# Kernel optimization log

Measured on AMD Instinct MI355X. Metric: run time of the kernel, lower is better.

## Reference

```python
import jax, jax.numpy as jnp
import numpy as np

D_MODEL = 1024
NUM_HEADS = 16
HEAD_DIM = D_MODEL // NUM_HEADS


def setup_inputs() -> dict:
    key = jax.random.key(0)
    k_x, k_wqkv, k_bqkv, k_wfc, k_bfc = jax.random.split(key, 5)
    scale_in = 1.0 / np.sqrt(D_MODEL)
    return {
        "x": jax.random.normal(k_x, (2, 2048, D_MODEL), dtype=jnp.float32),
        # torch nn.Linear stores weight as [out_features, in_features]
        "w_qkv": jax.random.uniform(k_wqkv, (3 * D_MODEL, D_MODEL), jnp.float32, -scale_in, scale_in),
        "b_qkv": jax.random.uniform(k_bqkv, (3 * D_MODEL,), jnp.float32, -scale_in, scale_in),
        "w_fc": jax.random.uniform(k_wfc, (D_MODEL, D_MODEL), jnp.float32, -scale_in, scale_in),
        "b_fc": jax.random.uniform(k_bfc, (D_MODEL,), jnp.float32, -scale_in, scale_in),
    }


def reference(x, w_qkv, b_qkv, w_fc, b_fc):
    B, S, _ = x.shape
    # fused QKV projection: [B,S,3*d_model]
    qkv = jnp.einsum("bsd,ed->bse", x, w_qkv) + b_qkv
    # [B,S,H,3*head_dim] -> [B,H,S,3*head_dim]
    qkv = qkv.reshape(B, S, NUM_HEADS, 3 * HEAD_DIM).transpose(0, 2, 1, 3)
    Q, K, V = jnp.split(qkv, 3, axis=-1)  # each [B,H,S,head_dim]
    scores = jnp.einsum("bhqd,bhkd->bhqk", Q, K) / np.sqrt(HEAD_DIM).astype(np.float32)
    attention = jax.nn.softmax(scores, axis=-1)  # [B,H,S,S]
    values = jnp.einsum("bhqk,bhkd->bhqd", attention, V)
    # [B,H,S,head_dim] -> [B,S,d_model]
    values = values.transpose(0, 2, 1, 3).reshape(B, S, D_MODEL)
    out = jnp.einsum("bsd,ed->bse", values, w_fc) + b_fc
    return out
```

## Files before the change

### kernel.cpp

```cpp
#include <hip/hip_runtime.h>
#include <hip/hip_bf16.h>

#define D_MODEL 1024
#define NH 16
#define HD 64
#define BATCH 2
#define SEQ 2048

typedef __attribute__((ext_vector_type(8))) short short8;
typedef __attribute__((ext_vector_type(4))) float floatx4;

static __device__ __forceinline__ short f2bf(float f) {
    __hip_bfloat16 h = __float2bfloat16(f);
    return *reinterpret_cast<short*>(&h);
}
static __device__ __forceinline__ unsigned int pk2bf(float a, float b) {
    float2 t; t.x = a; t.y = b;
    __hip_bfloat162 h2 = __float22bfloat162_rn(t);
    return *reinterpret_cast<unsigned int*>(&h2);
}

__global__ __launch_bounds__(256) void cvt_all(
    const float* __restrict__ x, const float* __restrict__ wq,
    const float* __restrict__ wf,
    short* __restrict__ Xb, short* __restrict__ Wqb, short* __restrict__ Wfb)
{
    int i = blockIdx.x * 256 + threadIdx.x;
    const float* src; short* dst; int off;
    if (i < 524288)      { src = x;  dst = Xb;  off = i; }
    else if (i < 917504) { src = wq; dst = Wqb; off = i - 524288; }
    else                 { src = wf; dst = Wfb; off = i - 917504; }
    float4 a = *reinterpret_cast<const float4*>(src + off * 8);
    float4 b = *reinterpret_cast<const float4*>(src + off * 8 + 4);
    short8 o;
    o[0] = f2bf(a.x); o[1] = f2bf(a.y); o[2] = f2bf(a.z); o[3] = f2bf(a.w);
    o[4] = f2bf(b.x); o[5] = f2bf(b.y); o[6] = f2bf(b.z); o[7] = f2bf(b.w);
    *reinterpret_cast<short8*>(dst + off * 8) = o;
}

__global__ __launch_bounds__(256) void qkv_gemm(
    const short* __restrict__ X, const short* __restrict__ W,
    const float* __restrict__ bias,
    short* __restrict__ Qs, short* __restrict__ Ks, short* __restrict__ Vt_g)
{
    __shared__ __align__(16) short As[128][72];
    __shared__ __align__(16) short Bs[64][72];
    const int tid = threadIdx.x;
    const int bx = blockIdx.x;
    const int m0 = blockIdx.y * 128;
    const int n0 = bx * 64;
    const int h = bx / 3, t = bx % 3;
    const int bi = m0 >> 11;
    const int sl0 = m0 & 2047;
    const int w = tid >> 6, lane = tid & 63;
    const int quad = lane >> 4, l15 = lane & 15;
    const int wm2 = w >> 1, wn2 = w & 1;

    floatx4 acc[4][2];
#pragma unroll
    for (int i = 0; i < 4; i++)
#pragma unroll
        for (int j = 0; j < 2; j++) acc[i][j] = (floatx4)0.0f;

    for (int k0 = 0; k0 < 1024; k0 += 64) {
        __syncthreads();
#pragma unroll
        for (int i = 0; i < 4; i++) {
            int c = tid + i * 256;
            int row = c >> 3, ck = c & 7;
            *reinterpret_cast<uint4*>(&As[row][ck * 8]) =
                *reinterpret_cast<const uint4*>(&X[(m0 + row) * 1024 + k0 + ck * 8]);
        }
#pragma unroll
        for (int i = 0; i < 2; i++) {
            int c = tid + i * 256;
            int row = c >> 3, ck = c & 7;
            *reinterpret_cast<uint4*>(&Bs[row][ck * 8]) =
                *reinterpret_cast<const uint4*>(&W[(n0 + row) * 1024 + k0 + ck * 8]);
        }
        __syncthreads();
#pragma unroll
        for (int kk = 0; kk < 2; kk++) {
            short8 a[4], b[2];
#pragma unroll
            for (int i = 0; i < 4; i++)
                a[i] = *reinterpret_cast<const short8*>(&As[wm2 * 64 + i * 16 + l15][kk * 32 + quad * 8]);
#pragma unroll
            for (int j = 0; j < 2; j++)
                b[j] = *reinterpret_cast<const short8*>(&Bs[wn2 * 32 + j * 16 + l15][kk * 32 + quad * 8]);
#pragma unroll
            for (int mt = 0; mt < 4; mt++)
#pragma unroll
                for (int nt = 0; nt < 2; nt++)
                    acc[mt][nt] = __builtin_amdgcn_mfma_f32_16x16x32_bf16(
                        a[mt], b[nt], acc[mt][nt], 0, 0, 0);
        }
    }

    __syncthreads();
    short* T = &As[0][0];
#pragma unroll
    for (int nt = 0; nt < 2; nt++) {
        int col = wn2 * 32 + nt * 16 + l15;
        float bv = bias[h * 192 + t * 64 + col];
#pragma unroll
        for (int mt = 0; mt < 4; mt++) {
#pragma unroll
            for (int r = 0; r < 4; r++) {
                int ml = wm2 * 64 + mt * 16 + quad * 4 + r;
                float v = acc[mt][nt][r] + bv;
                if (t == 0) v *= 0.125f;
                if (t < 2) As[ml][col] = f2bf(v);
                else       T[col * 136 + ml] = f2bf(v);
            }
        }
    }
    __syncthreads();

    if (t < 2) {
        short* dst = (t == 0) ? Qs : Ks;
#pragma unroll
        for (int i = 0; i < 4; i++) {
            int c = tid + i * 256;
            int row = c >> 3, ck = c & 7;
            uint4 u = *reinterpret_cast<const uint4*>(&As[row][ck * 8]);
            *reinterpret_cast<uint4*>(
                &dst[((size_t)(bi * NH + h) * SEQ + sl0 + row) * HD + ck * 8]) = u;
        }
    } else {
#pragma unroll
        for (int i = 0; i < 4; i++) {
            int c = tid + i * 256;
            int drow = c >> 4, ck = c & 15;
            uint4 u = *reinterpret_cast<const uint4*>(&T[drow * 136 + ck * 8]);
            *reinterpret_cast<uint4*>(
                &Vt_g[((size_t)(bi * NH + h) * HD + drow) * SEQ + sl0 + ck * 8]) = u;
        }
    }
}

__global__ __launch_bounds__(256) void attn_kernel(
    const short* __restrict__ Qs, const short* __restrict__ Ks,
    const short* __restrict__ Vt_g, short* __restrict__ attn)
{
    __shared__ __align__(16) char smem[64 * 72 * 2 * 2];
    __shared__ __align__(16) short Pl[4][32][40];
    __shared__ float Ls[2][64];

    short (*Kl)[72] = (short(*)[72])smem;
    short (*Vt)[72] = (short(*)[72])(smem + 64 * 72 * 2);
    float (*Osum)[66] = (float(*)[66])smem;

    const int tid = threadIdx.x;
    const int w = tid >> 6, lane = tid & 63;
    const int wq = w >> 1, wk = w & 1;
    const int quad = lane >> 4, l15 = lane & 15;
    const int q0 = blockIdx.x * 64;
    const int h = blockIdx.y, bi = blockIdx.z;
    const int bh = bi * NH + h;
    const int kbase = bh * SEQ * HD;
    const int vbase = bh * HD * SEQ;

    short8 aq[2][2];
#pragma unroll
    for (int qt2 = 0; qt2 < 2; qt2++) {
        const short* qp = Qs + kbase + (q0 + wq * 32 + qt2 * 16 + l15) * HD;
#pragma unroll
        for (int c = 0; c < 2; c++)
            aq[qt2][c] = *reinterpret_cast<const short8*>(qp + c * 32 + quad * 8);
    }

    float l_acc[2] = {0.f, 0.f};
    floatx4 o[2][4];
#pragma unroll
    for (int mt = 0; mt < 2; mt++)
#pragma unroll
        for (int nt = 0; nt < 4; nt++) o[mt][nt] = (floatx4)0.0f;

    for (int kt = 0; kt < SEQ; kt += 64) {
        __syncthreads();
#pragma unroll
        for (int i = 0; i < 2; i++) {
            int c = tid + i * 256;
            int row = c >> 3, ck = c & 7;
            *reinterpret_cast<uint4*>(&Kl[row][ck * 8]) =
                *reinterpret_cast<const uint4*>(&Ks[kbase + (kt + row) * HD + ck * 8]);
            *reinterpret_cast<uint4*>(&Vt[row][ck * 8]) =
                *reinterpret_cast<const uint4*>(&Vt_g[vbase + row * SEQ + kt + ck * 8]);
        }
        __syncthreads();

        floatx4 sf[2][2];
#pragma unroll
        for (int kt2 = 0; kt2 < 2; kt2++)
#pragma unroll
            for (int qt2 = 0; qt2 < 2; qt2++) sf[kt2][qt2] = (floatx4)0.0f;
#pragma unroll
        for (int c = 0; c < 2; c++) {
#pragma unroll
            for (int kt2 = 0; kt2 < 2; kt2++) {
                short8 bk = *reinterpret_cast<const short8*>(
                    &Kl[wk * 32 + kt2 * 16 + l15][c * 32 + quad * 8]);
#pragma unroll
                for (int qt2 = 0; qt2 < 2; qt2++)
                    sf[kt2][qt2] = __builtin_amdgcn_mfma_f32_16x16x32_bf16(
                        bk, aq[qt2][c], sf[kt2][qt2], 0, 0, 0);
            }
        }

#pragma unroll
        for (int kt2 = 0; kt2 < 2; kt2++) {
#pragma unroll
            for (int qt2 = 0; qt2 < 2; qt2++) {
                float e0 = __expf(sf[kt2][qt2][0]);
                float e1 = __expf(sf[kt2][qt2][1]);
                float e2 = __expf(sf[kt2][qt2][2]);
                float e3 = __expf(sf[kt2][qt2][3]);
                l_acc[qt2] += (e0 + e1) + (e2 + e3);
                uint2 p;
                p.x = pk2bf(e0, e1);
                p.y = pk2bf(e2, e3);
                *reinterpret_cast<uint2*>(&Pl[w][qt2 * 16 + l15][kt2 * 16 + quad * 4]) = p;
            }
        }
        asm volatile("s_waitcnt lgkmcnt(0)" ::: "memory");

#pragma unroll
        for (int mt = 0; mt < 2; mt++) {
            short8 ap = *reinterpret_cast<const short8*>(&Pl[w][mt * 16 + l15][quad * 8]);
#pragma unroll
            for (int nt = 0; nt < 4; nt++) {
                short8 bv = *reinterpret_cast<const short8*>(
                    &Vt[nt * 16 + l15][wk * 32 + quad * 8]);
                o[mt][nt] = __builtin_amdgcn_mfma_f32_16x16x32_bf16(
                    ap, bv, o[mt][nt], 0, 0, 0);
            }
        }
    }

#pragma unroll
    for (int qt2 = 0; qt2 < 2; qt2++) {
        l_acc[qt2] += __shfl_xor(l_acc[qt2], 16);
        l_acc[qt2] += __shfl_xor(l_acc[qt2], 32);
    }
    if (quad == 0) {
        Ls[wk][wq * 32 + l15]      = l_acc[0];
        Ls[wk][wq * 32 + 16 + l15] = l_acc[1];
    }
    __syncthreads();

    if (wk == 0) {
#pragma unroll
        for (int mt = 0; mt < 2; mt++)
#pragma unroll
            for (int nt = 0; nt < 4; nt++)
#pragma unroll
                for (int r = 0; r < 4; r++)
                    Osum[wq * 32 + mt * 16 + quad * 4 + r][nt * 16 + l15] = o[mt][nt][r];
    }
    __syncthreads();
    if (wk == 1) {
#pragma unroll
        for (int mt = 0; mt < 2; mt++) {
#pragma unroll
            for (int r = 0; r < 4; r++) {
                int qrow = wq * 32 + mt * 16 + quad * 4 + r;
                float lt = Ls[0][qrow] + Ls[1][qrow];
#pragma unroll
                for (int nt = 0; nt < 4; nt++) {
                    float val = (o[mt][nt][r] + Osum[qrow][nt * 16 + l15]) / lt;
                    attn[(bi * SEQ + q0 + qrow) * D_MODEL + h * HD + nt * 16 + l15] = f2bf(val);
                }
            }
        }
    }
}

__global__ __launch_bounds__(256) void fc_gemm(
    const short* __restrict__ A, const short* __restrict__ W,
    const float* __restrict__ bias, float* __restrict__ out)
{
    __shared__ __align__(16) short As[128][72];
    __shared__ __align__(16) short Bs[128][72];
    const int tid = threadIdx.x;
    const int m0 = blockIdx.y * 128;
    const int n0 = blockIdx.x * 128;
    const int w = tid >> 6, lane = tid & 63;
    const int quad = lane >> 4, l15 = lane & 15;
    const int wm = (w >> 1) * 64, wn = (w & 1) * 64;

    floatx4 acc[4][4];
#pragma unroll
    for (int i = 0; i < 4; i++)
#pragma unroll
        for (int j = 0; j < 4; j++) acc[i][j] = (floatx4)0.0f;

    for (int k0 = 0; k0 < 1024; k0 += 64) {
        __syncthreads();
#pragma unroll
        for (int i = 0; i < 4; i++) {
            int c = tid + i * 256;
            int row = c >> 3, ck = c & 7;
            *reinterpret_cast<uint4*>(&As[row][ck * 8]) =
                *reinterpret_cast<const uint4*>(&A[(m0 + row) * 1024 + k0 + ck * 8]);
            *reinterpret_cast<uint4*>(&Bs[row][ck * 8]) =
                *reinterpret_cast<const uint4*>(&W[(n0 + row) * 1024 + k0 + ck * 8]);
        }
        __syncthreads();
#pragma unroll
        for (int kk = 0; kk < 2; kk++) {
            short8 a[4], b[4];
#pragma unroll
            for (int t = 0; t < 4; t++) {
                a[t] = *reinterpret_cast<const short8*>(&As[wm + t * 16 + l15][kk * 32 + quad * 8]);
                b[t] = *reinterpret_cast<const short8*>(&Bs[wn + t * 16 + l15][kk * 32 + quad * 8]);
            }
#pragma unroll
            for (int mt = 0; mt < 4; mt++)
#pragma unroll
                for (int nt = 0; nt < 4; nt++)
                    acc[mt][nt] = __builtin_amdgcn_mfma_f32_16x16x32_bf16(
                        a[mt], b[nt], acc[mt][nt], 0, 0, 0);
        }
    }

#pragma unroll
    for (int nt = 0; nt < 4; nt++) {
        int col = n0 + wn + nt * 16 + l15;
        float bv = bias[col];
#pragma unroll
        for (int mt = 0; mt < 4; mt++) {
#pragma unroll
            for (int r = 0; r < 4; r++) {
                int row = m0 + wm + mt * 16 + quad * 4 + r;
                out[row * 1024 + col] = acc[mt][nt][r] + bv;
            }
        }
    }
}

extern "C" void kernel_launch(void* const* d_in, const int* in_sizes, int n_in,
                              void* d_out, int out_size, void* d_ws, size_t ws_size,
                              hipStream_t stream) {
    const float* x     = (const float*)d_in[0];
    const float* w_qkv = (const float*)d_in[1];
    const float* b_qkv = (const float*)d_in[2];
    const float* w_fc  = (const float*)d_in[3];
    const float* b_fc  = (const float*)d_in[4];
    float* out = (float*)d_out;

    const size_t M4 = 4u * 1024 * 1024;
    short* Xb    = (short*)d_ws;
    short* Wqb   = Xb + M4;
    short* Wfb   = Wqb + 3u * 1024 * 1024;
    short* Qs    = Wfb + 1024 * 1024;
    short* Ks    = Qs + M4;
    short* Vt_g  = Ks + M4;
    short* attnb = Xb;

    cvt_all<<<4096, 256, 0, stream>>>(x, w_qkv, w_fc, Xb, Wqb, Wfb);
    qkv_gemm<<<dim3(48, 32), 256, 0, stream>>>(Xb, Wqb, b_qkv, Qs, Ks, Vt_g);
    attn_kernel<<<dim3(32, 16, 2), 256, 0, stream>>>(Qs, Ks, Vt_g, attnb);
    fc_gemm<<<dim3(8, 32), 256, 0, stream>>>(attnb, Wfb, b_fc, out);
}
```

Baseline: 224.7 us.

## Give each attention warp full key range; halve fc_gemm N tile

The attention kernel now has each of the four warps own 32 query rows across the full 64-key tile, with 128 queries per block. This removes the split-K reduction across warp pairs through shared memory and its extra barriers, and halves the number of blocks so each K/V tile load is shared by twice as many queries. Separately, fc_gemm shrinks its N tile from 128 to 64, doubling the grid to 512 blocks to fill more CUs at the cost of reloading the A tiles more often. The attention change trades fewer blocks (512) and larger per-warp register and LDS use for less K/V traffic and simpler reduction.

```diff
diff --git a/kernel.cpp b/kernel.cpp
--- a/kernel.cpp
+++ b/kernel.cpp
@@ -143,19 +143,15 @@
     const short* __restrict__ Qs, const short* __restrict__ Ks,
     const short* __restrict__ Vt_g, short* __restrict__ attn)
 {
-    __shared__ __align__(16) char smem[64 * 72 * 2 * 2];
-    __shared__ __align__(16) short Pl[4][32][40];
-    __shared__ float Ls[2][64];
-
-    short (*Kl)[72] = (short(*)[72])smem;
-    short (*Vt)[72] = (short(*)[72])(smem + 64 * 72 * 2);
-    float (*Osum)[66] = (float(*)[66])smem;
+    __shared__ __align__(16) short Kl[64][72];
+    __shared__ __align__(16) short Vt[64][72];
+    __shared__ __align__(16) short Pl[4][32][72];
+    __shared__ float Ls[128];
 
     const int tid = threadIdx.x;
     const int w = tid >> 6, lane = tid & 63;
-    const int wq = w >> 1, wk = w & 1;
     const int quad = lane >> 4, l15 = lane & 15;
-    const int q0 = blockIdx.x * 64;
+    const int q0 = blockIdx.x * 128;
     const int h = blockIdx.y, bi = blockIdx.z;
     const int bh = bi * NH + h;
     const int kbase = bh * SEQ * HD;
@@ -164,7 +160,7 @@
     short8 aq[2][2];
 #pragma unroll
     for (int qt2 = 0; qt2 < 2; qt2++) {
-        const short* qp = Qs + kbase + (q0 + wq * 32 + qt2 * 16 + l15) * HD;
+        const short* qp = Qs + kbase + (q0 + w * 32 + qt2 * 16 + l15) * HD;
 #pragma unroll
         for (int c = 0; c < 2; c++)
             aq[qt2][c] = *reinterpret_cast<const short8*>(qp + c * 32 + quad * 8);
@@ -190,17 +186,17 @@
         }
         __syncthreads();
 
-        floatx4 sf[2][2];
-#pragma unroll
-        for (int kt2 = 0; kt2 < 2; kt2++)
+        floatx4 sf[4][2];
+#pragma unroll
+        for (int kt2 = 0; kt2 < 4; kt2++)
 #pragma unroll
             for (int qt2 = 0; qt2 < 2; qt2++) sf[kt2][qt2] = (floatx4)0.0f;
 #pragma unroll
         for (int c = 0; c < 2; c++) {
 #pragma unroll
-            for (int kt2 = 0; kt2 < 2; kt2++) {
+            for (int kt2 = 0; kt2 < 4; kt2++) {
                 short8 bk = *reinterpret_cast<const short8*>(
-                    &Kl[wk * 32 + kt2 * 16 + l15][c * 32 + quad * 8]);
+                    &Kl[kt2 * 16 + l15][c * 32 + quad * 8]);
 #pragma unroll
                 for (int qt2 = 0; qt2 < 2; qt2++)
                     sf[kt2][qt2] = __builtin_amdgcn_mfma_f32_16x16x32_bf16(
@@ -209,7 +205,7 @@
         }
 
 #pragma unroll
-        for (int kt2 = 0; kt2 < 2; kt2++) {
+        for (int kt2 = 0; kt2 < 4; kt2++) {
 #pragma unroll
             for (int qt2 = 0; qt2 < 2; qt2++) {
                 float e0 = __expf(sf[kt2][qt2][0]);
@@ -226,14 +222,18 @@
         asm volatile("s_waitcnt lgkmcnt(0)" ::: "memory");
 
 #pragma unroll
-        for (int mt = 0; mt < 2; mt++) {
-            short8 ap = *reinterpret_cast<const short8*>(&Pl[w][mt * 16 + l15][quad * 8]);
-#pragma unroll
-            for (int nt = 0; nt < 4; nt++) {
-                short8 bv = *reinterpret_cast<const short8*>(
-                    &Vt[nt * 16 + l15][wk * 32 + quad * 8]);
-                o[mt][nt] = __builtin_amdgcn_mfma_f32_16x16x32_bf16(
-                    ap, bv, o[mt][nt], 0, 0, 0);
+        for (int c = 0; c < 2; c++) {
+#pragma unroll
+            for (int mt = 0; mt < 2; mt++) {
+                short8 ap = *reinterpret_cast<const short8*>(
+                    &Pl[w][mt * 16 + l15][c * 32 + quad * 8]);
+#pragma unroll
+                for (int nt = 0; nt < 4; nt++) {
+                    short8 bv = *reinterpret_cast<const short8*>(
+                        &Vt[nt * 16 + l15][c * 32 + quad * 8]);
+                    o[mt][nt] = __builtin_amdgcn_mfma_f32_16x16x32_bf16(
+                        ap, bv, o[mt][nt], 0, 0, 0);
+                }
             }
         }
     }
@@ -244,33 +244,21 @@
         l_acc[qt2] += __shfl_xor(l_acc[qt2], 32);
     }
     if (quad == 0) {
-        Ls[wk][wq * 32 + l15]      = l_acc[0];
-        Ls[wk][wq * 32 + 16 + l15] = l_acc[1];
-    }
-    __syncthreads();
-
-    if (wk == 0) {
-#pragma unroll
-        for (int mt = 0; mt < 2; mt++)
-#pragma unroll
-            for (int nt = 0; nt < 4; nt++)
-#pragma unroll
-                for (int r = 0; r < 4; r++)
-                    Osum[wq * 32 + mt * 16 + quad * 4 + r][nt * 16 + l15] = o[mt][nt][r];
-    }
-    __syncthreads();
-    if (wk == 1) {
-#pragma unroll
-        for (int mt = 0; mt < 2; mt++) {
-#pragma unroll
-            for (int r = 0; r < 4; r++) {
-                int qrow = wq * 32 + mt * 16 + quad * 4 + r;
-                float lt = Ls[0][qrow] + Ls[1][qrow];
-#pragma unroll
-                for (int nt = 0; nt < 4; nt++) {
-                    float val = (o[mt][nt][r] + Osum[qrow][nt * 16 + l15]) / lt;
-                    attn[(bi * SEQ + q0 + qrow) * D_MODEL + h * HD + nt * 16 + l15] = f2bf(val);
-                }
+        Ls[w * 32 + l15] = l_acc[0];
+        Ls[w * 32 + 16 + l15] = l_acc[1];
+    }
+    asm volatile("s_waitcnt lgkmcnt(0)" ::: "memory");
+
+#pragma unroll
+    for (int mt = 0; mt < 2; mt++) {
+#pragma unroll
+        for (int r = 0; r < 4; r++) {
+            int ql = w * 32 + mt * 16 + quad * 4 + r;
+            float lt = Ls[ql];
+#pragma unroll
+            for (int nt = 0; nt < 4; nt++) {
+                attn[(bi * SEQ + q0 + ql) * D_MODEL + h * HD + nt * 16 + l15] =
+                    f2bf(o[mt][nt][r] / lt);
             }
         }
     }
@@ -281,19 +269,19 @@
     const float* __restrict__ bias, float* __restrict__ out)
 {
     __shared__ __align__(16) short As[128][72];
-    __shared__ __align__(16) short Bs[128][72];
+    __shared__ __align__(16) short Bs[64][72];
     const int tid = threadIdx.x;
     const int m0 = blockIdx.y * 128;
-    const int n0 = blockIdx.x * 128;
+    const int n0 = blockIdx.x * 64;
     const int w = tid >> 6, lane = tid & 63;
     const int quad = lane >> 4, l15 = lane & 15;
-    const int wm = (w >> 1) * 64, wn = (w & 1) * 64;
-
-    floatx4 acc[4][4];
+    const int wm2 = w >> 1, wn2 = w & 1;
+
+    floatx4 acc[4][2];
 #pragma unroll
     for (int i = 0; i < 4; i++)
 #pragma unroll
-        for (int j = 0; j < 4; j++) acc[i][j] = (floatx4)0.0f;
+        for (int j = 0; j < 2; j++) acc[i][j] = (floatx4)0.0f;
 
     for (int k0 = 0; k0 < 1024; k0 += 64) {
         __syncthreads();
@@ -303,36 +291,42 @@
             int row = c >> 3, ck = c & 7;
             *reinterpret_cast<uint4*>(&As[row][ck * 8]) =
                 *reinterpret_cast<const uint4*>(&A[(m0 + row) * 1024 + k0 + ck * 8]);
+        }
+#pragma unroll
+        for (int i = 0; i < 2; i++) {
+            int c = tid + i * 256;
+            int row = c >> 3, ck = c & 7;
             *reinterpret_cast<uint4*>(&Bs[row][ck * 8]) =
                 *reinterpret_cast<const uint4*>(&W[(n0 + row) * 1024 + k0 + ck * 8]);
         }
         __syncthreads();
 #pragma unroll
         for (int kk = 0; kk < 2; kk++) {
-            short8 a[4], b[4];
-#pragma unroll
-            for (int t = 0; t < 4; t++) {
-                a[t] = *reinterpret_cast<const short8*>(&As[wm + t * 16 + l15][kk * 32 + quad * 8]);
-                b[t] = *reinterpret_cast<const short8*>(&Bs[wn + t * 16 + l15][kk * 32 + quad * 8]);
-            }
+            short8 a[4], b[2];
+#pragma unroll
+            for (int i = 0; i < 4; i++)
+                a[i] = *reinterpret_cast<const short8*>(&As[wm2 * 64 + i * 16 + l15][kk * 32 + quad * 8]);
+#pragma unroll
+            for (int j = 0; j < 2; j++)
+                b[j] = *reinterpret_cast<const short8*>(&Bs[wn2 * 32 + j * 16 + l15][kk * 32 + quad * 8]);
 #pragma unroll
             for (int mt = 0; mt < 4; mt++)
 #pragma unroll
-                for (int nt = 0; nt < 4; nt++)
+                for (int nt = 0; nt < 2; nt++)
                     acc[mt][nt] = __builtin_amdgcn_mfma_f32_16x16x32_bf16(
                         a[mt], b[nt], acc[mt][nt], 0, 0, 0);
         }
     }
 
 #pragma unroll
-    for (int nt = 0; nt < 4; nt++) {
-        int col = n0 + wn + nt * 16 + l15;
+    for (int nt = 0; nt < 2; nt++) {
+        int col = n0 + wn2 * 32 + nt * 16 + l15;
         float bv = bias[col];
 #pragma unroll
         for (int mt = 0; mt < 4; mt++) {
 #pragma unroll
             for (int r = 0; r < 4; r++) {
-                int row = m0 + wm + mt * 16 + quad * 4 + r;
+                int row = m0 + wm2 * 64 + mt * 16 + quad * 4 + r;
                 out[row * 1024 + col] = acc[mt][nt][r] + bv;
             }
         }
@@ -360,6 +354,6 @@
 
     cvt_all<<<4096, 256, 0, stream>>>(x, w_qkv, w_fc, Xb, Wqb, Wfb);
     qkv_gemm<<<dim3(48, 32), 256, 0, stream>>>(Xb, Wqb, b_qkv, Qs, Ks, Vt_g);
-    attn_kernel<<<dim3(32, 16, 2), 256, 0, stream>>>(Qs, Ks, Vt_g, attnb);
-    fc_gemm<<<dim3(8, 32), 256, 0, stream>>>(attnb, Wfb, b_fc, out);
-}
+    attn_kernel<<<dim3(16, 16, 2), 256, 0, stream>>>(Qs, Ks, Vt_g, attnb);
+    fc_gemm<<<dim3(16, 32), 256, 0, stream>>>(attnb, Wfb, b_fc, out);
+}
```

Result: no change. 222.4 us (-1.1%).
